# Optimization experiments

Measured on AMD Instinct MI355X. Metric: run time of the kernel, lower is better.

## Reference

```python
import jax, jax.numpy as jnp
import numpy as np

ALPHA = 1.0
N, P, D = 8192, 128, 256
NUM_CLASSES = 128


def setup_inputs() -> dict:
    key = jax.random.key(0)
    kx, ky, kp = jax.random.split(key, 3)
    x = jax.random.normal(kx, (N, D), dtype=jnp.float32)
    y = jax.random.randint(ky, (N,), 0, NUM_CLASSES)
    prototypes = jax.random.normal(kp, (P, D), dtype=jnp.float32)
    return {"x": x, "y": y, "prototypes": prototypes}


def reference(x, y, prototypes):
    # (same math as the broadcasted sum((x-p)**2), expressed as a GEMM)
    x_sq = jnp.sum(x * x, axis=1, keepdims=True)          # [N, 1]
    p_sq = jnp.sum(prototypes * prototypes, axis=1)       # [P]
    dist = x_sq - 2.0 * jnp.einsum('nd,pd->np', x, prototypes) + p_sq[None, :]  # [N, P]

    # Torch code sets correct_mask[arange(N), y] = True, i.e. the "correct"
    # prototype is the one whose INDEX equals the class label y.
    n_idx = jnp.arange(dist.shape[0])
    d1 = dist[n_idx, y]                                    # [N] distance to correct prototype
    incorrect = jnp.where(jax.nn.one_hot(y, dist.shape[1], dtype=jnp.bool_),
                          jnp.inf, dist)
    d2 = jnp.min(incorrect, axis=1)                        # [N] min over wrong prototypes

    mu = (d1 - d2) / (d1 + d2)
    return jnp.mean(jax.nn.sigmoid(-ALPHA * mu))
```

## Files before the change

### kernel.cpp

```cpp
#include <hip/hip_runtime.h>
#include <math.h>

#define N_ROWS  8192
#define DIM     256
#define NPROTO  128

typedef float f32x4 __attribute__((ext_vector_type(4)));
typedef short s16x8 __attribute__((ext_vector_type(8)));

__device__ __forceinline__ unsigned short f2bf(float f) {
  unsigned int u = __float_as_uint(f);
  u += 0x7fffu + ((u >> 16) & 1u);
  return (unsigned short)(u >> 16);
}

__device__ __forceinline__ void gl_lds16(const void* g, void* l) {
  __builtin_amdgcn_global_load_lds(
      (const __attribute__((address_space(1))) void*)g,
      (__attribute__((address_space(3))) void*)l, 16, 0, 0);
}

__global__ __launch_bounds__(256) void glvq_prep(
    const float* __restrict__ x, const float* __restrict__ proto,
    unsigned short* __restrict__ xbf, float* __restrict__ xsq,
    unsigned short* __restrict__ pbf, float* __restrict__ psq,
    float* __restrict__ out) {
  const int t = threadIdx.x;
  const int b = blockIdx.x;

  {
    const int r = b * 16 + (t >> 4);
    const int i = t & 15;
    const float4* xr = (const float4*)x + (size_t)r * 64 + i * 4;
    float4 v0 = xr[0], v1 = xr[1], v2 = xr[2], v3 = xr[3];
    union { s16x8 v; unsigned short u[8]; } pk0, pk1;
    pk0.u[0] = f2bf(v0.x); pk0.u[1] = f2bf(v0.y); pk0.u[2] = f2bf(v0.z); pk0.u[3] = f2bf(v0.w);
    pk0.u[4] = f2bf(v1.x); pk0.u[5] = f2bf(v1.y); pk0.u[6] = f2bf(v1.z); pk0.u[7] = f2bf(v1.w);
    pk1.u[0] = f2bf(v2.x); pk1.u[1] = f2bf(v2.y); pk1.u[2] = f2bf(v2.z); pk1.u[3] = f2bf(v2.w);
    pk1.u[4] = f2bf(v3.x); pk1.u[5] = f2bf(v3.y); pk1.u[6] = f2bf(v3.z); pk1.u[7] = f2bf(v3.w);
    *(s16x8*)&xbf[(size_t)r * 256 + i * 16] = pk0.v;
    *(s16x8*)&xbf[(size_t)r * 256 + i * 16 + 8] = pk1.v;
    float s = v0.x * v0.x + v0.y * v0.y + v0.z * v0.z + v0.w * v0.w +
              v1.x * v1.x + v1.y * v1.y + v1.z * v1.z + v1.w * v1.w +
              v2.x * v2.x + v2.y * v2.y + v2.z * v2.z + v2.w * v2.w +
              v3.x * v3.x + v3.y * v3.y + v3.z * v3.z + v3.w * v3.w;
#pragma unroll
    for (int m = 1; m <= 8; m <<= 1) s += __shfl_xor(s, m);
    if (i == 0) xsq[r] = s;
  }

  if (b < 16) {
    const int tid = b * 256 + t;
    const int row = tid >> 5;
    const int co  = tid & 31;
    const float4* p4 = (const float4*)proto;
    float4 a = p4[tid * 2];
    float4 bb = p4[tid * 2 + 1];
    union { s16x8 v; unsigned short u[8]; } pk;
    pk.u[0] = f2bf(a.x);  pk.u[1] = f2bf(a.y);  pk.u[2] = f2bf(a.z);  pk.u[3] = f2bf(a.w);
    pk.u[4] = f2bf(bb.x); pk.u[5] = f2bf(bb.y); pk.u[6] = f2bf(bb.z); pk.u[7] = f2bf(bb.w);
    const int slot = row * 32 + (co ^ (row & 7));
    *(s16x8*)&pbf[slot * 8] = pk.v;
    float s = a.x * a.x + a.y * a.y + a.z * a.z + a.w * a.w +
              bb.x * bb.x + bb.y * bb.y + bb.z * bb.z + bb.w * bb.w;
#pragma unroll
    for (int m = 1; m <= 16; m <<= 1) s += __shfl_xor(s, m);
    if (co == 0) psq[row] = s;
  }
  if (b == 0 && t == 0) out[0] = 0.f;
}

__global__ __launch_bounds__(128) void glvq_main(
    const unsigned short* __restrict__ xbf, const float* __restrict__ xsq_g,
    const int* __restrict__ y, const unsigned short* __restrict__ pbf,
    const float* __restrict__ psq_g, float* __restrict__ out) {
  __shared__ unsigned short pT[NPROTO * 256];

  const int t = threadIdx.x;
#pragma unroll
  for (int j = 0; j < 32; ++j) {
    const int c = j * 128 + t;
    gl_lds16((const char*)pbf + (size_t)c * 16, (char*)pT + (size_t)c * 16);
  }

  const int wv = t >> 6, l = t & 63, mq = l >> 4, mc = l & 15;
  const int row_base = blockIdx.x * 32 + wv * 16;

  float xs[4]; int yr[4];
#pragma unroll
  for (int reg = 0; reg < 4; ++reg) {
    xs[reg] = xsq_g[row_base + mq * 4 + reg];
    yr[reg] = y[row_base + mq * 4 + reg];
  }
  float pq[8];
#pragma unroll
  for (int j = 0; j < 8; ++j) pq[j] = psq_g[j * 16 + mc];

  s16x8 afr[8];
  const unsigned short* xrow = xbf + (size_t)(row_base + mc) * 256;
#pragma unroll
  for (int ks = 0; ks < 8; ++ks)
    afr[ks] = *(const s16x8*)(xrow + ks * 32 + mq * 8);

  __syncthreads();

  f32x4 acc[8];
#pragma unroll
  for (int j = 0; j < 8; ++j) acc[j] = (f32x4){0.f, 0.f, 0.f, 0.f};
  const int m7 = mc & 7;
#pragma unroll
  for (int ks = 0; ks < 8; ++ks) {
#pragma unroll
    for (int j = 0; j < 8; ++j) {
      const int p = j * 16 + mc;
      const s16x8 bf = *(const s16x8*)&pT[(p * 32 + ((4 * ks + mq) ^ m7)) * 8];
      acc[j] = __builtin_amdgcn_mfma_f32_16x16x32_bf16(afr[ks], bf, acc[j], 0, 0, 0);
    }
  }

  float ssum = 0.f;
#pragma unroll
  for (int reg = 0; reg < 4; ++reg) {
    float d1 = 1e30f, d2 = 1e30f;
#pragma unroll
    for (int j = 0; j < 8; ++j) {
      const float d = xs[reg] + pq[j] - 2.f * acc[j][reg];
      if (j * 16 + mc == yr[reg]) d1 = d; else d2 = fminf(d2, d);
    }
#pragma unroll
    for (int m = 1; m <= 8; m <<= 1) {
      d1 = fminf(d1, __shfl_xor(d1, m));
      d2 = fminf(d2, __shfl_xor(d2, m));
    }
    const float mu = (d1 - d2) / (d1 + d2);
    ssum += 1.f / (1.f + __expf(mu));
  }
  if (mc != 0) ssum = 0.f;
  ssum += __shfl_xor(ssum, 16);
  ssum += __shfl_xor(ssum, 32);
  if (l == 0) atomicAdd(out, ssum * (1.f / (float)N_ROWS));
}

extern "C" void kernel_launch(void* const* d_in, const int* in_sizes, int n_in,
                              void* d_out, int out_size, void* d_ws, size_t ws_size,
                              hipStream_t stream) {
  const float* x = (const float*)d_in[0];
  const int* y = (const int*)d_in[1];
  const float* proto = (const float*)d_in[2];
  float* out = (float*)d_out;

  char* ws = (char*)d_ws;
  unsigned short* pbf = (unsigned short*)ws;
  unsigned short* xbf = (unsigned short*)(ws + 65536);
  float* xsq = (float*)(ws + 65536 + (size_t)N_ROWS * DIM * 2);
  float* psq = (float*)(ws + 65536 + (size_t)N_ROWS * DIM * 2 + N_ROWS * 4);

  glvq_prep<<<512, 256, 0, stream>>>(x, proto, xbf, xsq, pbf, psq, out);
  glvq_main<<<256, 128, 0, stream>>>(xbf, xsq, y, pbf, psq, out);
}
```

Baseline: 71.90 us.

## Fuse x bf16 conversion and row norms into main GEMM kernel

The x conversion to bf16 and the squared-norm computation move from the prep kernel into the main kernel. The main kernel now reads fp32 x directly into MFMA A fragments and gets each row norm with lane shuffles. This removes the 4 MB bf16 round trip through global memory and shrinks the prep kernel to 16 blocks that only handle the prototypes. In exchange the main kernel reads twice as many bytes per row and has more conversion ALU work before its MFMA loop.

```diff
diff --git a/kernel.cpp b/kernel.cpp
--- a/kernel.cpp
+++ b/kernel.cpp
@@ -21,59 +21,31 @@
 }
 
 __global__ __launch_bounds__(256) void glvq_prep(
-    const float* __restrict__ x, const float* __restrict__ proto,
-    unsigned short* __restrict__ xbf, float* __restrict__ xsq,
-    unsigned short* __restrict__ pbf, float* __restrict__ psq,
-    float* __restrict__ out) {
-  const int t = threadIdx.x;
-  const int b = blockIdx.x;
-
-  {
-    const int r = b * 16 + (t >> 4);
-    const int i = t & 15;
-    const float4* xr = (const float4*)x + (size_t)r * 64 + i * 4;
-    float4 v0 = xr[0], v1 = xr[1], v2 = xr[2], v3 = xr[3];
-    union { s16x8 v; unsigned short u[8]; } pk0, pk1;
-    pk0.u[0] = f2bf(v0.x); pk0.u[1] = f2bf(v0.y); pk0.u[2] = f2bf(v0.z); pk0.u[3] = f2bf(v0.w);
-    pk0.u[4] = f2bf(v1.x); pk0.u[5] = f2bf(v1.y); pk0.u[6] = f2bf(v1.z); pk0.u[7] = f2bf(v1.w);
-    pk1.u[0] = f2bf(v2.x); pk1.u[1] = f2bf(v2.y); pk1.u[2] = f2bf(v2.z); pk1.u[3] = f2bf(v2.w);
-    pk1.u[4] = f2bf(v3.x); pk1.u[5] = f2bf(v3.y); pk1.u[6] = f2bf(v3.z); pk1.u[7] = f2bf(v3.w);
-    *(s16x8*)&xbf[(size_t)r * 256 + i * 16] = pk0.v;
-    *(s16x8*)&xbf[(size_t)r * 256 + i * 16 + 8] = pk1.v;
-    float s = v0.x * v0.x + v0.y * v0.y + v0.z * v0.z + v0.w * v0.w +
-              v1.x * v1.x + v1.y * v1.y + v1.z * v1.z + v1.w * v1.w +
-              v2.x * v2.x + v2.y * v2.y + v2.z * v2.z + v2.w * v2.w +
-              v3.x * v3.x + v3.y * v3.y + v3.z * v3.z + v3.w * v3.w;
+    const float* __restrict__ proto, unsigned short* __restrict__ pbf,
+    float* __restrict__ psq, float* __restrict__ out) {
+  const int tid = blockIdx.x * 256 + threadIdx.x;
+  const int row = tid >> 5;
+  const int co  = tid & 31;
+  const float4* p4 = (const float4*)proto;
+  float4 a = p4[tid * 2];
+  float4 b = p4[tid * 2 + 1];
+  union { s16x8 v; unsigned short u[8]; } pk;
+  pk.u[0] = f2bf(a.x); pk.u[1] = f2bf(a.y); pk.u[2] = f2bf(a.z); pk.u[3] = f2bf(a.w);
+  pk.u[4] = f2bf(b.x); pk.u[5] = f2bf(b.y); pk.u[6] = f2bf(b.z); pk.u[7] = f2bf(b.w);
+  const int slot = row * 32 + (co ^ (row & 7));
+  *(s16x8*)&pbf[slot * 8] = pk.v;
+  float s = a.x * a.x + a.y * a.y + a.z * a.z + a.w * a.w +
+            b.x * b.x + b.y * b.y + b.z * b.z + b.w * b.w;
 #pragma unroll
-    for (int m = 1; m <= 8; m <<= 1) s += __shfl_xor(s, m);
-    if (i == 0) xsq[r] = s;
-  }
-
-  if (b < 16) {
-    const int tid = b * 256 + t;
-    const int row = tid >> 5;
-    const int co  = tid & 31;
-    const float4* p4 = (const float4*)proto;
-    float4 a = p4[tid * 2];
-    float4 bb = p4[tid * 2 + 1];
-    union { s16x8 v; unsigned short u[8]; } pk;
-    pk.u[0] = f2bf(a.x);  pk.u[1] = f2bf(a.y);  pk.u[2] = f2bf(a.z);  pk.u[3] = f2bf(a.w);
-    pk.u[4] = f2bf(bb.x); pk.u[5] = f2bf(bb.y); pk.u[6] = f2bf(bb.z); pk.u[7] = f2bf(bb.w);
-    const int slot = row * 32 + (co ^ (row & 7));
-    *(s16x8*)&pbf[slot * 8] = pk.v;
-    float s = a.x * a.x + a.y * a.y + a.z * a.z + a.w * a.w +
-              bb.x * bb.x + bb.y * bb.y + bb.z * bb.z + bb.w * bb.w;
-#pragma unroll
-    for (int m = 1; m <= 16; m <<= 1) s += __shfl_xor(s, m);
-    if (co == 0) psq[row] = s;
-  }
-  if (b == 0 && t == 0) out[0] = 0.f;
+  for (int m = 1; m <= 16; m <<= 1) s += __shfl_xor(s, m);
+  if (co == 0) psq[row] = s;
+  if (tid == 0) out[0] = 0.f;
 }
 
 __global__ __launch_bounds__(128) void glvq_main(
-    const unsigned short* __restrict__ xbf, const float* __restrict__ xsq_g,
-    const int* __restrict__ y, const unsigned short* __restrict__ pbf,
-    const float* __restrict__ psq_g, float* __restrict__ out) {
+    const float* __restrict__ x, const int* __restrict__ y,
+    const unsigned short* __restrict__ pbf, const float* __restrict__ psq_g,
+    float* __restrict__ out) {
   __shared__ unsigned short pT[NPROTO * 256];
 
   const int t = threadIdx.x;
@@ -86,21 +58,34 @@
   const int wv = t >> 6, l = t & 63, mq = l >> 4, mc = l & 15;
   const int row_base = blockIdx.x * 32 + wv * 16;
 
+  s16x8 afr[8];
+  float sx = 0.f;
+  {
+    const float4* xr = (const float4*)x + (size_t)(row_base + mc) * 64;
+#pragma unroll
+    for (int ks = 0; ks < 8; ++ks) {
+      float4 a = xr[ks * 8 + mq * 2];
+      float4 b = xr[ks * 8 + mq * 2 + 1];
+      union { s16x8 v; unsigned short u[8]; } pk;
+      pk.u[0] = f2bf(a.x); pk.u[1] = f2bf(a.y); pk.u[2] = f2bf(a.z); pk.u[3] = f2bf(a.w);
+      pk.u[4] = f2bf(b.x); pk.u[5] = f2bf(b.y); pk.u[6] = f2bf(b.z); pk.u[7] = f2bf(b.w);
+      afr[ks] = pk.v;
+      sx += a.x * a.x + a.y * a.y + a.z * a.z + a.w * a.w +
+            b.x * b.x + b.y * b.y + b.z * b.z + b.w * b.w;
+    }
+  }
+  sx += __shfl_xor(sx, 16);
+  sx += __shfl_xor(sx, 32);
   float xs[4]; int yr[4];
+  const int yv = y[row_base + mc];
 #pragma unroll
   for (int reg = 0; reg < 4; ++reg) {
-    xs[reg] = xsq_g[row_base + mq * 4 + reg];
-    yr[reg] = y[row_base + mq * 4 + reg];
+    xs[reg] = __shfl(sx, mq * 4 + reg);
+    yr[reg] = __shfl(yv, mq * 4 + reg);
   }
   float pq[8];
 #pragma unroll
   for (int j = 0; j < 8; ++j) pq[j] = psq_g[j * 16 + mc];
-
-  s16x8 afr[8];
-  const unsigned short* xrow = xbf + (size_t)(row_base + mc) * 256;
-#pragma unroll
-  for (int ks = 0; ks < 8; ++ks)
-    afr[ks] = *(const s16x8*)(xrow + ks * 32 + mq * 8);
 
   __syncthreads();
 
@@ -149,12 +134,9 @@
   const float* proto = (const float*)d_in[2];
   float* out = (float*)d_out;
 
-  char* ws = (char*)d_ws;
-  unsigned short* pbf = (unsigned short*)ws;
-  unsigned short* xbf = (unsigned short*)(ws + 65536);
-  float* xsq = (float*)(ws + 65536 + (size_t)N_ROWS * DIM * 2);
-  float* psq = (float*)(ws + 65536 + (size_t)N_ROWS * DIM * 2 + N_ROWS * 4);
+  unsigned short* pbf = (unsigned short*)d_ws;
+  float* psq = (float*)((char*)d_ws + NPROTO * DIM * 2);
 
-  glvq_prep<<<512, 256, 0, stream>>>(x, proto, xbf, xsq, pbf, psq, out);
-  glvq_main<<<256, 128, 0, stream>>>(xbf, xsq, y, pbf, psq, out);
+  glvq_prep<<<16, 256, 0, stream>>>(proto, pbf, psq, out);
+  glvq_main<<<256, 128, 0, stream>>>(x, y, pbf, psq, out);
 }
```

Result: no change. 71.22 us (-1.0%).
